# Performance work log

Hardware: AMD Instinct MI355X
Metric: run time of the kernel (lower is better)

Reference implementation:

```python
import jax, jax.numpy as jnp
import numpy as np

N = 32768   # num nodes
E = 65536   # num edges
H = 64      # hidden_size
EH = 64     # edge_hidden_size
LN_EPS = 1e-5


def setup_inputs() -> dict:
    key = jax.random.key(0)
    ks = jax.random.split(key, 6)
    node_emb = jax.random.normal(ks[0], (N, H), dtype=jnp.float32)
    edge_emb = jax.random.normal(ks[1], (E, EH), dtype=jnp.float32)
    edge_index = jax.random.randint(ks[2], (2, E), 0, N, dtype=jnp.int64)
    # edge_weight_net MLP: edge_hidden -> hidden (relu) -> H*H, xavier-uniform style scales
    W1 = jax.random.normal(ks[3], (EH, H), dtype=jnp.float32) * (2.0 / (EH + H)) ** 0.5
    b1 = jnp.zeros((H,), dtype=jnp.float32)
    W2 = jax.random.normal(ks[4], (H, H * H), dtype=jnp.float32) * (2.0 / (H + H * H)) ** 0.5
    b2 = jnp.zeros((H * H,), dtype=jnp.float32)
    root = jax.random.normal(ks[5], (H, H), dtype=jnp.float32) * (2.0 / (H + H)) ** 0.5
    bias = jnp.zeros((H,), dtype=jnp.float32)
    gamma = jnp.ones((H,), dtype=jnp.float32)
    beta = jnp.zeros((H,), dtype=jnp.float32)
    return {"node_emb": node_emb, "edge_emb": edge_emb, "W1": W1, "b1": b1,
            "W2": W2, "b2": b2, "root": root, "bias": bias,
            "gamma": gamma, "beta": beta, "edge_index": edge_index}


def reference(node_emb, edge_emb, W1, b1, W2, b2, root, bias, gamma, beta, edge_index):
    src, dst = edge_index[0], edge_index[1]
    num_nodes = node_emb.shape[0]
    # edge-conditioned weight: MLP(edge_emb) -> per-edge [H, H] matrix ('full' mode)
    h = jax.nn.relu(edge_emb @ W1 + b1)                 # [E, H]
    W = (h @ W2 + b2).reshape(-1, H, H)                 # [E, H, H]
    # message = x_src @ W_e  (bmm of [1,H] x [H,H] per edge)
    msg = jnp.einsum('eh,ehk->ek', node_emb[src], W)    # [E, H]
    # scatter-add aggregation at destination nodes
    agg = jax.ops.segment_sum(msg, dst, num_segments=num_nodes)          # [N, H]
    deg = jax.ops.segment_sum(jnp.ones_like(dst, dtype=node_emb.dtype), dst,
                              num_segments=num_nodes)                    # [N]
    agg = agg / jnp.maximum(deg, 1.0)[:, None]          # 'mean' aggregation
    # root transform + bias + residual
    out = agg + node_emb @ root + bias + node_emb       # [N, H]
    # LayerNorm over hidden dim
    mu = jnp.mean(out, axis=-1, keepdims=True)
    var = jnp.var(out, axis=-1, keepdims=True)
    out = (out - mu) * jax.lax.rsqrt(var + LN_EPS) * gamma + beta
    return out
```

## Files before the change

### kernel.cpp

```cpp
#include <hip/hip_runtime.h>

#define N_NODES 32768
#define N_EDGES 65536

typedef _Float16 f16;
typedef _Float16 f16x8 __attribute__((ext_vector_type(8)));
typedef float f32x16 __attribute__((ext_vector_type(16)));

#define WS_AGG   0
#define WS_DEG   8388608
#define WS_W2    8519680
#define WS_W1    9109504
#define WS_ROOT  9117696

__device__ inline f16 u16_as_f16(unsigned short u) {
  union { unsigned short s; f16 h; } v; v.s = u; return v.h;
}
__device__ inline f16x8 splat8(f16 x) {
  f16x8 r;
  #pragma unroll
  for (int u = 0; u < 8; ++u) r[u] = x;
  return r;
}
__device__ inline f16x8 cvt8(float4 p0, float4 p1) {
  f16x8 a;
  a[0] = (f16)p0.x; a[1] = (f16)p0.y; a[2] = (f16)p0.z; a[3] = (f16)p0.w;
  a[4] = (f16)p1.x; a[5] = (f16)p1.y; a[6] = (f16)p1.z; a[7] = (f16)p1.w;
  return a;
}

__global__ __launch_bounds__(256) void k_prep(const float* __restrict__ W1,
                                              const float* __restrict__ W2,
                                              const float* __restrict__ b2,
                                              const float* __restrict__ root,
                                              const int* __restrict__ eidx,
                                              float* __restrict__ deg,
                                              char* __restrict__ w2v2,
                                              char* __restrict__ w1v2,
                                              char* __restrict__ rootv2) {
  int t = blockIdx.x * 256 + threadIdx.x;
  if (t < 294912) {
    int col = t & 63, h = (t >> 6) & 63, j = t >> 12;
    float v = 0.f;
    if (j < 64)       v = W2[j * 4096 + h * 64 + col];
    else if (j == 64) v = b2[h * 64 + col];
    int oct = j * 8 + (h >> 4) * 2 + ((h >> 3) & 1);
    *(f16*)(w2v2 + oct * 1024 + col * 16 + (h & 7) * 2) = (f16)v;
  } else if (t < 299008) {
    int u2 = t - 294912; int col = u2 & 63, i = u2 >> 6;
    int oct = (i >> 4) * 2 + ((i >> 3) & 1);
    *(f16*)(w1v2 + oct * 1024 + col * 16 + (i & 7) * 2) = (f16)W1[i * 64 + col];
  } else if (t < 303104) {
    int u2 = t - 299008; int col = u2 & 63, i = u2 >> 6;
    int oct = (i >> 4) * 2 + ((i >> 3) & 1);
    *(f16*)(rootv2 + oct * 1024 + col * 16 + (i & 7) * 2) = (f16)root[i * 64 + col];
  } else if (t < 368640) {
    int e = t - 303104;
    unsafeAtomicAdd(&deg[eidx[N_EDGES + e]], 1.0f);
  }
}

__global__ __launch_bounds__(512, 2) void k_main(const float* __restrict__ node,
                                                 const float* __restrict__ edge,
                                                 const float* __restrict__ b1,
                                                 const int* __restrict__ eidx,
                                                 const char* __restrict__ w2v2,
                                                 const char* __restrict__ w1v2,
                                                 float* __restrict__ agg) {
  extern __shared__ char smem[];
  char* ldsH = smem + 65536;

  const int tid = threadIdx.x;
  const int lane = tid & 63;
  const int wv = tid >> 6;
  const int ln31 = lane & 31;
  const int half = lane >> 5;
  const int ebase = blockIdx.x * 256;

  {
    const int e = ebase + wv * 32 + ln31;
    const float4* er = (const float4*)edge + (long)e * 16;
    f32x16 c0 = {}, c1 = {};
    #pragma unroll
    for (int kk = 0; kk < 4; ++kk) {
      f16x8 a = cvt8(er[kk * 4 + half * 2], er[kk * 4 + half * 2 + 1]);
      f16x8 bf0 = *(const f16x8*)(w1v2 + (kk * 2 + half) * 1024 + ln31 * 16);
      f16x8 bf1 = *(const f16x8*)(w1v2 + (kk * 2 + half) * 1024 + 512 + ln31 * 16);
      c0 = __builtin_amdgcn_mfma_f32_32x32x16_f16(a, bf0, c0, 0, 0, 0);
      c1 = __builtin_amdgcn_mfma_f32_32x32x16_f16(a, bf1, c1, 0, 0, 0);
    }
    const float bb0 = b1[ln31], bb1 = b1[32 + ln31];
    char* hb = ldsH + wv * 4864;
    #pragma unroll
    for (int r = 0; r < 16; ++r) {
      const int m = (r & 3) + 8 * (r >> 2) + 4 * half;
      *(f16*)(hb + m * 152 + ln31 * 2)      = (f16)fmaxf(c0[r] + bb0, 0.f);
      *(f16*)(hb + m * 152 + 64 + ln31 * 2) = (f16)fmaxf(c1[r] + bb1, 0.f);
    }
    if (half == 0) {
      *(uint2*)(hb + ln31 * 152 + 128) = make_uint2(0x00003C00u, 0u);
      *(uint2*)(hb + ln31 * 152 + 136) = make_uint2(0u, 0u);
    }
  }

  const int g = wv >> 1;
  const int ch = wv & 1;
  f16x8 xf[2][4];
  #pragma unroll
  for (int t = 0; t < 2; ++t) {
    const int e = ebase + (2 * g + t) * 32 + ln31;
    const int s = eidx[e];
    const float4* xr = (const float4*)node + (long)s * 16;
    #pragma unroll
    for (int kk = 0; kk < 4; ++kk)
      xf[t][kk] = cvt8(xr[kk * 4 + half * 2], xr[kk * 4 + half * 2 + 1]);
  }

  const uint4* w2p = (const uint4*)w2v2;
  uint4 st0 = w2p[tid], st1 = w2p[512 + tid], st2 = w2p[1024 + tid], st3 = w2p[1536 + tid];

  f32x16 accA = {}, accB = {};
  const char* hA = ldsH + (2 * g) * 4864 + ln31 * 152;
  const char* hB = ldsH + (2 * g + 1) * 4864 + ln31 * 152;

  __syncthreads();

  for (int c = 0; c < 17; ++c) {
    char* buf = smem + (c & 1) * 32768;
    *(uint4*)(buf + tid * 16)         = st0;
    *(uint4*)(buf + 8192 + tid * 16)  = st1;
    *(uint4*)(buf + 16384 + tid * 16) = st2;
    *(uint4*)(buf + 24576 + tid * 16) = st3;
    if (c < 16) {
      const uint4* src = w2p + (c + 1) * 2048;
      st0 = src[tid]; st1 = src[512 + tid]; st2 = src[1024 + tid]; st3 = src[1536 + tid];
    }
    __syncthreads();
    const uint2 hAv = *(const uint2*)(hA + c * 8);
    const uint2 hBv = *(const uint2*)(hB + c * 8);
    #pragma unroll
    for (int j = 0; j < 4; ++j) {
      const unsigned short ua = (unsigned short)((j < 2 ? (hAv.x >> (j * 16)) : (hAv.y >> ((j - 2) * 16))) & 0xffffu);
      const unsigned short ub = (unsigned short)((j < 2 ? (hBv.x >> (j * 16)) : (hBv.y >> ((j - 2) * 16))) & 0xffffu);
      const f16x8 haS = splat8(u16_as_f16(ua));
      const f16x8 hbS = splat8(u16_as_f16(ub));
      #pragma unroll
      for (int kk = 0; kk < 4; ++kk) {
        const f16x8 bf = *(const f16x8*)(buf + (j * 8 + kk * 2 + half) * 1024 + ch * 512 + ln31 * 16);
        accA = __builtin_amdgcn_mfma_f32_32x32x16_f16(xf[0][kk] * haS, bf, accA, 0, 0, 0);
        accB = __builtin_amdgcn_mfma_f32_32x32x16_f16(xf[1][kk] * hbS, bf, accB, 0, 0, 0);
      }
    }
  }

  #pragma unroll
  for (int t = 0; t < 2; ++t) {
    const int base = ebase + (2 * g + t) * 32;
    #pragma unroll
    for (int r = 0; r < 16; ++r) {
      const int m = (r & 3) + 8 * (r >> 2) + 4 * half;
      const int d = eidx[N_EDGES + base + m];
      const float v = (t == 0) ? accA[r] : accB[r];
      unsafeAtomicAdd(&agg[(long)d * 64 + ch * 32 + ln31], v);
    }
  }
}

__global__ __launch_bounds__(256) void k_node(const float* __restrict__ node,
                                              const float* __restrict__ agg,
                                              const float* __restrict__ deg,
                                              const char* __restrict__ rootv2,
                                              const float* __restrict__ bias,
                                              const float* __restrict__ gamma,
                                              const float* __restrict__ beta,
                                              float* __restrict__ out) {
  const int tid = threadIdx.x;
  const int lane = tid & 63;
  const int wv = tid >> 6;
  const int ln31 = lane & 31;
  const int half = lane >> 5;
  const int nb = blockIdx.x * 128 + wv * 32;

  f32x16 c0 = {}, c1 = {};
  const float4* xr = (const float4*)node + (long)(nb + ln31) * 16;
  #pragma unroll
  for (int kk = 0; kk < 4; ++kk) {
    f16x8 a = cvt8(xr[kk * 4 + half * 2], xr[kk * 4 + half * 2 + 1]);
    f16x8 b0 = *(const f16x8*)(rootv2 + (kk * 2 + half) * 1024 + ln31 * 16);
    f16x8 b1f = *(const f16x8*)(rootv2 + (kk * 2 + half) * 1024 + 512 + ln31 * 16);
    c0 = __builtin_amdgcn_mfma_f32_32x32x16_f16(a, b0, c0, 0, 0, 0);
    c1 = __builtin_amdgcn_mfma_f32_32x32x16_f16(a, b1f, c1, 0, 0, 0);
  }
  const float bi0 = bias[ln31],  bi1 = bias[32 + ln31];
  const float g0  = gamma[ln31], g1  = gamma[32 + ln31];
  const float be0 = beta[ln31],  be1 = beta[32 + ln31];
  #pragma unroll
  for (int r = 0; r < 16; ++r) {
    const int m = (r & 3) + 8 * (r >> 2) + 4 * half;
    const int n = nb + m;
    const float rd = 1.f / fmaxf(deg[n], 1.f);
    const float pre0 = agg[n * 64 + ln31] * rd + c0[r] + bi0 + node[n * 64 + ln31];
    const float pre1 = agg[n * 64 + 32 + ln31] * rd + c1[r] + bi1 + node[n * 64 + 32 + ln31];
    float s = pre0 + pre1, s2 = pre0 * pre0 + pre1 * pre1;
    #pragma unroll
    for (int mk = 16; mk >= 1; mk >>= 1) {
      s  += __shfl_xor(s, mk, 64);
      s2 += __shfl_xor(s2, mk, 64);
    }
    const float mu  = s * 0.015625f;
    const float var = s2 * 0.015625f - mu * mu;
    const float inv = rsqrtf(var + 1e-5f);
    out[n * 64 + ln31]      = (pre0 - mu) * inv * g0 + be0;
    out[n * 64 + 32 + ln31] = (pre1 - mu) * inv * g1 + be1;
  }
}

extern "C" void kernel_launch(void* const* d_in, const int* in_sizes, int n_in,
                              void* d_out, int out_size, void* d_ws, size_t ws_size,
                              hipStream_t stream) {
  const float* node  = (const float*)d_in[0];
  const float* edgee = (const float*)d_in[1];
  const float* W1    = (const float*)d_in[2];
  const float* b1    = (const float*)d_in[3];
  const float* W2    = (const float*)d_in[4];
  const float* b2    = (const float*)d_in[5];
  const float* root  = (const float*)d_in[6];
  const float* bias  = (const float*)d_in[7];
  const float* gamma = (const float*)d_in[8];
  const float* beta  = (const float*)d_in[9];
  const int*   eidx  = (const int*)d_in[10];
  float* out = (float*)d_out;

  char* ws = (char*)d_ws;
  float* agg    = (float*)(ws + WS_AGG);
  float* deg    = (float*)(ws + WS_DEG);
  char*  w2v2   = ws + WS_W2;
  char*  w1v2   = ws + WS_W1;
  char*  rootv2 = ws + WS_ROOT;

  hipMemsetAsync(ws, 0, 8519680, stream);

  k_prep<<<1440, 256, 0, stream>>>(W1, W2, b2, root, eidx, deg, w2v2, w1v2, rootv2);

  hipFuncSetAttribute((const void*)k_main, hipFuncAttributeMaxDynamicSharedMemorySize, 104448);
  k_main<<<256, 512, 104448, stream>>>(node, edgee, b1, eidx, w2v2, w1v2, agg);

  k_node<<<256, 256, 0, stream>>>(node, agg, deg, rootv2, bias, gamma, beta, out);
}
```

Baseline: 149.3 us.

## Stream W2 fragments directly into registers with 4 edge tiles per wave

The main kernel no longer stages W2 chunks through double-buffered LDS with block-wide barriers. Each wave now loads its W2 fragments straight from global/L2 into registers, software-pipelined across two buffers, and processes 4 edge tiles instead of 2 so every loaded fragment feeds more MFMAs. The b2 term becomes a final unscaled MFMA instead of a padded h=1 column. The residual is folded into the root matrix as root+I, which drops one node load in the epilogue. Blocks shrink to 256 threads with lower occupancy and higher register pressure, and all waves now read W2 from cache.

```diff
diff --git a/kernel.cpp b/kernel.cpp
--- a/kernel.cpp
+++ b/kernel.cpp
@@ -10,8 +10,10 @@
 #define WS_AGG   0
 #define WS_DEG   8388608
 #define WS_W2    8519680
-#define WS_W1    9109504
-#define WS_ROOT  9117696
+#define WS_W1    9060352
+#define WS_ROOT  9068544
+
+#define MFMA(a, b, c) __builtin_amdgcn_mfma_f32_32x32x16_f16((a), (b), (c), 0, 0, 0)
 
 __device__ inline f16 u16_as_f16(unsigned short u) {
   union { unsigned short s; f16 h; } v; v.s = u; return v.h;
@@ -37,38 +39,42 @@
                                               float* __restrict__ deg,
                                               char* __restrict__ w2v2,
                                               char* __restrict__ w1v2,
-                                              char* __restrict__ rootv2) {
+                                              char* __restrict__ rootIv2) {
   int t = blockIdx.x * 256 + threadIdx.x;
-  if (t < 294912) {
-    int col = t & 63, h = (t >> 6) & 63, j = t >> 12;
+  if (t < 270336) {
+    int oct = t >> 9, q = t & 511;
+    int col = q >> 3, hl = q & 7;
+    int j = oct >> 3, sub = oct & 7;
+    int h = (sub >> 1) * 16 + (sub & 1) * 8 + hl;
     float v = 0.f;
     if (j < 64)       v = W2[j * 4096 + h * 64 + col];
     else if (j == 64) v = b2[h * 64 + col];
-    int oct = j * 8 + (h >> 4) * 2 + ((h >> 3) & 1);
-    *(f16*)(w2v2 + oct * 1024 + col * 16 + (h & 7) * 2) = (f16)v;
-  } else if (t < 299008) {
-    int u2 = t - 294912; int col = u2 & 63, i = u2 >> 6;
-    int oct = (i >> 4) * 2 + ((i >> 3) & 1);
-    *(f16*)(w1v2 + oct * 1024 + col * 16 + (i & 7) * 2) = (f16)W1[i * 64 + col];
-  } else if (t < 303104) {
-    int u2 = t - 299008; int col = u2 & 63, i = u2 >> 6;
-    int oct = (i >> 4) * 2 + ((i >> 3) & 1);
-    *(f16*)(rootv2 + oct * 1024 + col * 16 + (i & 7) * 2) = (f16)root[i * 64 + col];
-  } else if (t < 368640) {
-    int e = t - 303104;
+    *(f16*)(w2v2 + t * 2) = (f16)v;
+  } else if (t < 274432) {
+    int u = t - 270336;
+    int oct = u >> 9, q = u & 511, col = q >> 3, hl = q & 7;
+    int i = (oct >> 1) * 16 + (oct & 1) * 8 + hl;
+    *(f16*)(w1v2 + u * 2) = (f16)W1[i * 64 + col];
+  } else if (t < 278528) {
+    int u = t - 274432;
+    int oct = u >> 9, q = u & 511, col = q >> 3, hl = q & 7;
+    int i = (oct >> 1) * 16 + (oct & 1) * 8 + hl;
+    float v = root[i * 64 + col] + (i == col ? 1.f : 0.f);
+    *(f16*)(rootIv2 + u * 2) = (f16)v;
+  } else if (t < 344064) {
+    int e = t - 278528;
     unsafeAtomicAdd(&deg[eidx[N_EDGES + e]], 1.0f);
   }
 }
 
-__global__ __launch_bounds__(512, 2) void k_main(const float* __restrict__ node,
+__global__ __launch_bounds__(256, 1) void k_main(const float* __restrict__ node,
                                                  const float* __restrict__ edge,
                                                  const float* __restrict__ b1,
                                                  const int* __restrict__ eidx,
                                                  const char* __restrict__ w2v2,
                                                  const char* __restrict__ w1v2,
                                                  float* __restrict__ agg) {
-  extern __shared__ char smem[];
-  char* ldsH = smem + 65536;
+  __shared__ char ldsH[34816];
 
   const int tid = threadIdx.x;
   const int lane = tid & 63;
@@ -77,38 +83,38 @@
   const int half = lane >> 5;
   const int ebase = blockIdx.x * 256;
 
-  {
-    const int e = ebase + wv * 32 + ln31;
+  const char* w1p = w1v2 + half * 1024 + ln31 * 16;
+  #pragma unroll
+  for (int t = 0; t < 2; ++t) {
+    const int tile = 2 * wv + t;
+    const int e = ebase + tile * 32 + ln31;
     const float4* er = (const float4*)edge + (long)e * 16;
     f32x16 c0 = {}, c1 = {};
     #pragma unroll
     for (int kk = 0; kk < 4; ++kk) {
       f16x8 a = cvt8(er[kk * 4 + half * 2], er[kk * 4 + half * 2 + 1]);
-      f16x8 bf0 = *(const f16x8*)(w1v2 + (kk * 2 + half) * 1024 + ln31 * 16);
-      f16x8 bf1 = *(const f16x8*)(w1v2 + (kk * 2 + half) * 1024 + 512 + ln31 * 16);
-      c0 = __builtin_amdgcn_mfma_f32_32x32x16_f16(a, bf0, c0, 0, 0, 0);
-      c1 = __builtin_amdgcn_mfma_f32_32x32x16_f16(a, bf1, c1, 0, 0, 0);
+      f16x8 bf0 = *(const f16x8*)(w1p + (kk * 2 << 10));
+      f16x8 bf1 = *(const f16x8*)(w1p + (kk * 2 << 10) + 512);
+      c0 = MFMA(a, bf0, c0);
+      c1 = MFMA(a, bf1, c1);
     }
     const float bb0 = b1[ln31], bb1 = b1[32 + ln31];
-    char* hb = ldsH + wv * 4864;
+    char* hb = ldsH + tile * 32 * 136;
     #pragma unroll
     for (int r = 0; r < 16; ++r) {
       const int m = (r & 3) + 8 * (r >> 2) + 4 * half;
-      *(f16*)(hb + m * 152 + ln31 * 2)      = (f16)fmaxf(c0[r] + bb0, 0.f);
-      *(f16*)(hb + m * 152 + 64 + ln31 * 2) = (f16)fmaxf(c1[r] + bb1, 0.f);
-    }
-    if (half == 0) {
-      *(uint2*)(hb + ln31 * 152 + 128) = make_uint2(0x00003C00u, 0u);
-      *(uint2*)(hb + ln31 * 152 + 136) = make_uint2(0u, 0u);
-    }
-  }
-
-  const int g = wv >> 1;
+      *(f16*)(hb + m * 136 + ln31 * 2)      = (f16)fmaxf(c0[r] + bb0, 0.f);
+      *(f16*)(hb + m * 136 + 64 + ln31 * 2) = (f16)fmaxf(c1[r] + bb1, 0.f);
+    }
+  }
+
   const int ch = wv & 1;
-  f16x8 xf[2][4];
-  #pragma unroll
-  for (int t = 0; t < 2; ++t) {
-    const int e = ebase + (2 * g + t) * 32 + ln31;
+  const int g  = wv >> 1;
+
+  f16x8 xf[4][4];
+  #pragma unroll
+  for (int t = 0; t < 4; ++t) {
+    const int e = ebase + (g * 4 + t) * 32 + ln31;
     const int s = eidx[e];
     const float4* xr = (const float4*)node + (long)s * 16;
     #pragma unroll
@@ -116,52 +122,80 @@
       xf[t][kk] = cvt8(xr[kk * 4 + half * 2], xr[kk * 4 + half * 2 + 1]);
   }
 
-  const uint4* w2p = (const uint4*)w2v2;
-  uint4 st0 = w2p[tid], st1 = w2p[512 + tid], st2 = w2p[1024 + tid], st3 = w2p[1536 + tid];
-
-  f32x16 accA = {}, accB = {};
-  const char* hA = ldsH + (2 * g) * 4864 + ln31 * 152;
-  const char* hB = ldsH + (2 * g + 1) * 4864 + ln31 * 152;
+  const char* wp = w2v2 + half * 1024 + ch * 512 + ln31 * 16;
+  f16x8 bufA[8], bufB[8];
+  #pragma unroll
+  for (int jj = 0; jj < 2; ++jj)
+    #pragma unroll
+    for (int kk = 0; kk < 4; ++kk)
+      bufA[jj * 4 + kk] = *(const f16x8*)(wp + ((jj * 8 + kk * 2) << 10));
+
+  f32x16 acc[4] = {};
+  const char* hp[4];
+  #pragma unroll
+  for (int t = 0; t < 4; ++t) hp[t] = ldsH + (g * 128 + t * 32 + ln31) * 136;
 
   __syncthreads();
 
-  for (int c = 0; c < 17; ++c) {
-    char* buf = smem + (c & 1) * 32768;
-    *(uint4*)(buf + tid * 16)         = st0;
-    *(uint4*)(buf + 8192 + tid * 16)  = st1;
-    *(uint4*)(buf + 16384 + tid * 16) = st2;
-    *(uint4*)(buf + 24576 + tid * 16) = st3;
-    if (c < 16) {
-      const uint4* src = w2p + (c + 1) * 2048;
-      st0 = src[tid]; st1 = src[512 + tid]; st2 = src[1024 + tid]; st3 = src[1536 + tid];
-    }
-    __syncthreads();
-    const uint2 hAv = *(const uint2*)(hA + c * 8);
-    const uint2 hBv = *(const uint2*)(hB + c * 8);
-    #pragma unroll
-    for (int j = 0; j < 4; ++j) {
-      const unsigned short ua = (unsigned short)((j < 2 ? (hAv.x >> (j * 16)) : (hAv.y >> ((j - 2) * 16))) & 0xffffu);
-      const unsigned short ub = (unsigned short)((j < 2 ? (hBv.x >> (j * 16)) : (hBv.y >> ((j - 2) * 16))) & 0xffffu);
-      const f16x8 haS = splat8(u16_as_f16(ua));
-      const f16x8 hbS = splat8(u16_as_f16(ub));
-      #pragma unroll
-      for (int kk = 0; kk < 4; ++kk) {
-        const f16x8 bf = *(const f16x8*)(buf + (j * 8 + kk * 2 + half) * 1024 + ch * 512 + ln31 * 16);
-        accA = __builtin_amdgcn_mfma_f32_32x32x16_f16(xf[0][kk] * haS, bf, accA, 0, 0, 0);
-        accB = __builtin_amdgcn_mfma_f32_32x32x16_f16(xf[1][kk] * hbS, bf, accB, 0, 0, 0);
-      }
-    }
-  }
-
-  #pragma unroll
-  for (int t = 0; t < 2; ++t) {
-    const int base = ebase + (2 * g + t) * 32;
+  for (int cp = 0; cp < 16; ++cp) {
+    const char* base = wp + (cp << 15);
+    uint2 hv[4];
+    #pragma unroll
+    for (int t = 0; t < 4; ++t) hv[t] = *(const uint2*)(hp[t] + cp * 8);
+
+    #pragma unroll
+    for (int jj = 0; jj < 2; ++jj)
+      #pragma unroll
+      for (int kk = 0; kk < 4; ++kk)
+        bufB[jj * 4 + kk] = *(const f16x8*)(base + 16384 + ((jj * 8 + kk * 2) << 10));
+
+    #pragma unroll
+    for (int jj = 0; jj < 2; ++jj) {
+      f16x8 sp[4];
+      #pragma unroll
+      for (int t = 0; t < 4; ++t)
+        sp[t] = splat8(u16_as_f16((unsigned short)(hv[t].x >> (jj * 16))));
+      #pragma unroll
+      for (int kk = 0; kk < 4; ++kk)
+        #pragma unroll
+        for (int t = 0; t < 4; ++t)
+          acc[t] = MFMA(xf[t][kk] * sp[t], bufA[jj * 4 + kk], acc[t]);
+    }
+
+    #pragma unroll
+    for (int jj = 0; jj < 2; ++jj)
+      #pragma unroll
+      for (int kk = 0; kk < 4; ++kk)
+        bufA[jj * 4 + kk] = *(const f16x8*)(base + 32768 + ((jj * 8 + kk * 2) << 10));
+
+    #pragma unroll
+    for (int jj = 0; jj < 2; ++jj) {
+      f16x8 sp[4];
+      #pragma unroll
+      for (int t = 0; t < 4; ++t)
+        sp[t] = splat8(u16_as_f16((unsigned short)(hv[t].y >> (jj * 16))));
+      #pragma unroll
+      for (int kk = 0; kk < 4; ++kk)
+        #pragma unroll
+        for (int t = 0; t < 4; ++t)
+          acc[t] = MFMA(xf[t][kk] * sp[t], bufB[jj * 4 + kk], acc[t]);
+    }
+  }
+
+  #pragma unroll
+  for (int kk = 0; kk < 4; ++kk)
+    #pragma unroll
+    for (int t = 0; t < 4; ++t)
+      acc[t] = MFMA(xf[t][kk], bufA[kk], acc[t]);
+
+  #pragma unroll
+  for (int t = 0; t < 4; ++t) {
+    const int base_e = ebase + (g * 4 + t) * 32;
     #pragma unroll
     for (int r = 0; r < 16; ++r) {
       const int m = (r & 3) + 8 * (r >> 2) + 4 * half;
-      const int d = eidx[N_EDGES + base + m];
-      const float v = (t == 0) ? accA[r] : accB[r];
-      unsafeAtomicAdd(&agg[(long)d * 64 + ch * 32 + ln31], v);
+      const int d = eidx[N_EDGES + base_e + m];
+      unsafeAtomicAdd(&agg[(long)d * 64 + ch * 32 + ln31], acc[t][r]);
     }
   }
 }
@@ -169,7 +203,7 @@
 __global__ __launch_bounds__(256) void k_node(const float* __restrict__ node,
                                               const float* __restrict__ agg,
                                               const float* __restrict__ deg,
-                                              const char* __restrict__ rootv2,
+                                              const char* __restrict__ rootIv2,
                                               const float* __restrict__ bias,
                                               const float* __restrict__ gamma,
                                               const float* __restrict__ beta,
@@ -181,15 +215,16 @@
   const int half = lane >> 5;
   const int nb = blockIdx.x * 128 + wv * 32;
 
+  const char* rp = rootIv2 + half * 1024 + ln31 * 16;
   f32x16 c0 = {}, c1 = {};
   const float4* xr = (const float4*)node + (long)(nb + ln31) * 16;
   #pragma unroll
   for (int kk = 0; kk < 4; ++kk) {
     f16x8 a = cvt8(xr[kk * 4 + half * 2], xr[kk * 4 + half * 2 + 1]);
-    f16x8 b0 = *(const f16x8*)(rootv2 + (kk * 2 + half) * 1024 + ln31 * 16);
-    f16x8 b1f = *(const f16x8*)(rootv2 + (kk * 2 + half) * 1024 + 512 + ln31 * 16);
-    c0 = __builtin_amdgcn_mfma_f32_32x32x16_f16(a, b0, c0, 0, 0, 0);
-    c1 = __builtin_amdgcn_mfma_f32_32x32x16_f16(a, b1f, c1, 0, 0, 0);
+    f16x8 b0 = *(const f16x8*)(rp + (kk * 2 << 10));
+    f16x8 b1f = *(const f16x8*)(rp + (kk * 2 << 10) + 512);
+    c0 = MFMA(a, b0, c0);
+    c1 = MFMA(a, b1f, c1);
   }
   const float bi0 = bias[ln31],  bi1 = bias[32 + ln31];
   const float g0  = gamma[ln31], g1  = gamma[32 + ln31];
@@ -199,8 +234,8 @@
     const int m = (r & 3) + 8 * (r >> 2) + 4 * half;
     const int n = nb + m;
     const float rd = 1.f / fmaxf(deg[n], 1.f);
-    const float pre0 = agg[n * 64 + ln31] * rd + c0[r] + bi0 + node[n * 64 + ln31];
-    const float pre1 = agg[n * 64 + 32 + ln31] * rd + c1[r] + bi1 + node[n * 64 + 32 + ln31];
+    const float pre0 = agg[n * 64 + ln31] * rd + c0[r] + bi0;
+    const float pre1 = agg[n * 64 + 32 + ln31] * rd + c1[r] + bi1;
     float s = pre0 + pre1, s2 = pre0 * pre0 + pre1 * pre1;
     #pragma unroll
     for (int mk = 16; mk >= 1; mk >>= 1) {
@@ -232,18 +267,15 @@
   float* out = (float*)d_out;
 
   char* ws = (char*)d_ws;
-  float* agg    = (float*)(ws + WS_AGG);
-  float* deg    = (float*)(ws + WS_DEG);
-  char*  w2v2   = ws + WS_W2;
-  char*  w1v2   = ws + WS_W1;
-  char*  rootv2 = ws + WS_ROOT;
+  float* agg     = (float*)(ws + WS_AGG);
+  float* deg     = (float*)(ws + WS_DEG);
+  char*  w2v2    = ws + WS_W2;
+  char*  w1v2    = ws + WS_W1;
+  char*  rootIv2 = ws + WS_ROOT;
 
   hipMemsetAsync(ws, 0, 8519680, stream);
 
-  k_prep<<<1440, 256, 0, stream>>>(W1, W2, b2, root, eidx, deg, w2v2, w1v2, rootv2);
-
-  hipFuncSetAttribute((const void*)k_main, hipFuncAttributeMaxDynamicSharedMemorySize, 104448);
-  k_main<<<256, 512, 104448, stream>>>(node, edgee, b1, eidx, w2v2, w1v2, agg);
-
-  k_node<<<256, 256, 0, stream>>>(node, agg, deg, rootv2, bias, gamma, beta, out);
-}
+  k_prep<<<1344, 256, 0, stream>>>(W1, W2, b2, root, eidx, deg, w2v2, w1v2, rootIv2);
+  k_main<<<256, 256, 0, stream>>>(node, edgee, b1, eidx, w2v2, w1v2, agg);
+  k_node<<<256, 256, 0, stream>>>(node, agg, deg, rootIv2, bias, gamma, beta, out);
+}
```

New measurement: 143.4 us. 1.04x faster.
